# Kernel tuning notes

Measured on AMD Instinct MI355X. Metric: run time of the kernel, lower is better.

The kernel has to match this reference:

```python
import jax, jax.numpy as jnp
import numpy as np

BN_EPS = 1e-5


def gcn_conv(x, src, dst, n, W, b):
    # PyG GCNConv: h = x @ W; add self-loops; symmetric deg^{-1/2} norm; scatter-add; + bias
    h = x @ W
    sl = jnp.arange(n, dtype=src.dtype)
    src_f = jnp.concatenate([src, sl])
    dst_f = jnp.concatenate([dst, sl])
    deg = jax.ops.segment_sum(jnp.ones_like(dst_f, dtype=h.dtype), dst_f, num_segments=n)
    dis = jnp.where(deg > 0, jax.lax.rsqrt(jnp.maximum(deg, 1.0)), 0.0)
    norm = dis[src_f] * dis[dst_f]                       # [E+N]
    msg = h[src_f] * norm[:, None]                       # gather + scale
    out = jax.ops.segment_sum(msg, dst_f, num_segments=n)  # scatter-add
    return out + b


def batchnorm(x, g, b):
    # training-mode BatchNorm1d (batch statistics), deterministic
    mu = jnp.mean(x, axis=0)
    var = jnp.mean((x - mu) ** 2, axis=0)
    return g * (x - mu) * jax.lax.rsqrt(var + BN_EPS) + b


def setup_inputs() -> dict:
    key = jax.random.key(0)
    ks = jax.random.split(key, 12)
    N, E, F_IN, D, M, G = 40000, 640000, 128, 128, 256, 2000
    x = jax.random.normal(ks[0], (N, F_IN), dtype=jnp.float32)
    edge_index = jax.random.randint(ks[1], (2, E), 0, N, dtype=jnp.int64)
    batch = jnp.sort(jax.random.randint(ks[2], (N,), 0, G, dtype=jnp.int64))
    s = lambda fi: 1.0 / np.sqrt(fi)
    W1 = jax.random.normal(ks[3], (F_IN, D), dtype=jnp.float32) * s(F_IN)
    b1 = jnp.zeros((D,), jnp.float32)
    W2 = jax.random.normal(ks[4], (D, D), dtype=jnp.float32) * s(D)
    b2 = jnp.zeros((D,), jnp.float32)
    bn1_g = jnp.ones((D,), jnp.float32); bn1_b = jnp.zeros((D,), jnp.float32)
    bn2_g = jnp.ones((D,), jnp.float32); bn2_b = jnp.zeros((D,), jnp.float32)
    fc1_w = jax.random.normal(ks[5], (D, M), dtype=jnp.float32) * s(D)
    fc1_b = jnp.zeros((M,), jnp.float32)
    fc2_w = jax.random.normal(ks[6], (M, M), dtype=jnp.float32) * s(M)
    fc2_b = jnp.zeros((M,), jnp.float32)
    fc3_w = jax.random.normal(ks[7], (M, 1), dtype=jnp.float32) * s(M)
    fc3_b = jnp.zeros((1,), jnp.float32)
    return dict(x=x, edge_index=edge_index, batch=batch, num_graphs=G,
                W1=W1, b1=b1, W2=W2, b2=b2,
                bn1_g=bn1_g, bn1_b=bn1_b, bn2_g=bn2_g, bn2_b=bn2_b,
                fc1_w=fc1_w, fc1_b=fc1_b, fc2_w=fc2_w, fc2_b=fc2_b,
                fc3_w=fc3_w, fc3_b=fc3_b)


def reference(x, edge_index, batch, num_graphs, W1, b1, W2, b2,
              bn1_g, bn1_b, bn2_g, bn2_b,
              fc1_w, fc1_b, fc2_w, fc2_b, fc3_w, fc3_b):
    n = x.shape[0]
    src, dst = edge_index[0], edge_index[1]
    h = gcn_conv(x, src, dst, n, W1, b1)
    h = jax.nn.relu(batchnorm(h, bn1_g, bn1_b))
    h = gcn_conv(h, src, dst, n, W2, b2)
    h = jax.nn.relu(batchnorm(h, bn2_g, bn2_b))
    g = jax.ops.segment_sum(h, batch, num_segments=num_graphs)  # scatter_sum pooling [G, D]
    g = jax.nn.relu(g @ fc1_w + fc1_b)   # dropout is identity in eval
    g = jax.nn.relu(g @ fc2_w + fc2_b)
    return g @ fc3_w + fc3_b             # [G, 1]
```

## Files before the change

kernel.cpp:

```cpp
#include <hip/hip_runtime.h>
#include <hip/hip_fp16.h>

#define NN 40000
#define NE 640000
#define DF 128
#define NG 2000
#define NCH 157
#define CNTB 625
#define G1_BLKS 313
#define NDPAD 40192

typedef unsigned int u32;
typedef __attribute__((ext_vector_type(8))) short short8;
typedef __attribute__((ext_vector_type(4))) float floatx4;

__device__ inline float2 bf2_to_f2(u32 u) {
    return make_float2(__uint_as_float(u << 16), __uint_as_float(u & 0xffff0000u));
}
__device__ inline u32 f_to_bf(float f) {
    u32 u = __float_as_uint(f);
    return (u + 0x7fffu + ((u >> 16) & 1u)) >> 16;
}
__device__ inline u32 pack_bf2(float a, float b) {
    return f_to_bf(a) | (f_to_bf(b) << 16);
}
__device__ inline float bf_to_f(short s) {
    return __uint_as_float(((u32)(unsigned short)s) << 16);
}
__device__ inline float colw_to_f(int cw) {
    return __half2float(__ushort_as_half((unsigned short)((u32)cw >> 16)));
}

template<bool BF16IN, bool FUSE_BN, bool WT_F32, bool TILE128>
__device__ __forceinline__ void gemm_core(const void* __restrict__ Xv, const void* __restrict__ wsrc,
                                          u32* __restrict__ outb, const float* __restrict__ slots,
                                          const float* __restrict__ gam, const float* __restrict__ bet,
                                          int bid, char* sbuf, float* sc, float* sh) {
    unsigned short* wlds = (unsigned short*)sbuf;
    unsigned short* clds = (unsigned short*)sbuf;
    int tid = threadIdx.x;
    int row0 = bid * (TILE128 ? 128 : 64);

    if (FUSE_BN) {
        if (tid < 128) {
            float s = 0.f, q = 0.f;
            for (int k = 0; k < 64; k++) {
                s += slots[k * 256 + tid];
                q += slots[k * 256 + 128 + tid];
            }
            const float inv_n = 1.0f / (float)NN;
            float mu = s * inv_n;
            float va = fmaf(-mu, mu, q * inv_n);
            float a = gam[tid] * rsqrtf(va + 1e-5f);
            sc[tid] = a;
            sh[tid] = fmaf(-mu, a, bet[tid]);
        }
    }
    if (WT_F32) {
        const float* W = (const float*)wsrc;
        for (int i = tid; i < 16384; i += 256) {
            int k = i >> 7, c = i & 127;
            wlds[c * 136 + k] = (unsigned short)f_to_bf(W[i]);
        }
    } else {
        const unsigned short* wt = (const unsigned short*)wsrc;
        for (int i = tid; i < 2048; i += 256) {
            int c = i >> 4, s = i & 15;
            *(uint4*)&wlds[c * 136 + s * 8] = ((const uint4*)wt)[i];
        }
    }
    __syncthreads();

    int lane = tid & 63;
    int wave = tid >> 6;
    int qr = lane >> 4;
    int rl = lane & 15;

    if (TILE128) {
        int rA0 = row0 + wave * 32 + rl;
        int rA1 = rA0 + 16;
        int rA0c = rA0 < NN ? rA0 : NN - 1;
        int rA1c = rA1 < NN ? rA1 : NN - 1;
        floatx4 acc[2][8];
#pragma unroll
        for (int a = 0; a < 2; a++)
#pragma unroll
            for (int b = 0; b < 8; b++) acc[a][b] = (floatx4){0.f, 0.f, 0.f, 0.f};
#pragma unroll
        for (int kb = 0; kb < 4; kb++) {
            int k0 = kb * 32 + qr * 8;
            short8 a0, a1;
            if (!BF16IN) {
                const float* p0 = (const float*)Xv + (size_t)rA0c * DF + k0;
                const float* p1 = (const float*)Xv + (size_t)rA1c * DF + k0;
                float4 u0 = *(const float4*)p0, u1 = *(const float4*)(p0 + 4);
                float4 v0 = *(const float4*)p1, v1 = *(const float4*)(p1 + 4);
                float fa[8] = {u0.x, u0.y, u0.z, u0.w, u1.x, u1.y, u1.z, u1.w};
                float fb[8] = {v0.x, v0.y, v0.z, v0.w, v1.x, v1.y, v1.z, v1.w};
#pragma unroll
                for (int j = 0; j < 8; j++) { a0[j] = (short)f_to_bf(fa[j]); a1[j] = (short)f_to_bf(fb[j]); }
            } else {
                a0 = *(const short8*)((const u32*)Xv + (size_t)rA0c * 64 + (k0 >> 1));
                a1 = *(const short8*)((const u32*)Xv + (size_t)rA1c * 64 + (k0 >> 1));
                if (FUSE_BN) {
#pragma unroll
                    for (int j = 0; j < 8; j++) {
                        float f0 = fmaxf(fmaf(bf_to_f(a0[j]), sc[k0 + j], sh[k0 + j]), 0.f);
                        float f1 = fmaxf(fmaf(bf_to_f(a1[j]), sc[k0 + j], sh[k0 + j]), 0.f);
                        a0[j] = (short)f_to_bf(f0);
                        a1[j] = (short)f_to_bf(f1);
                    }
                }
            }
#pragma unroll
            for (int ct = 0; ct < 8; ct++) {
                short8 bfr = *(const short8*)&wlds[(ct * 16 + rl) * 136 + k0];
                acc[0][ct] = __builtin_amdgcn_mfma_f32_16x16x32_bf16(a0, bfr, acc[0][ct], 0, 0, 0);
                acc[1][ct] = __builtin_amdgcn_mfma_f32_16x16x32_bf16(a1, bfr, acc[1][ct], 0, 0, 0);
            }
        }
        __syncthreads();
#pragma unroll
        for (int rt = 0; rt < 2; rt++)
#pragma unroll
            for (int ct = 0; ct < 8; ct++)
#pragma unroll
                for (int r = 0; r < 4; r++) {
                    int lr = wave * 32 + rt * 16 + qr * 4 + r;
                    int c = ct * 16 + rl;
                    clds[lr * 136 + c] = (unsigned short)f_to_bf(acc[rt][ct][r]);
                }
        __syncthreads();
        for (int i = tid; i < 2048; i += 256) {
            int lr = i >> 4, s = i & 15;
            int grow = row0 + lr;
            if (grow < NN) {
                uint4 v = *(const uint4*)&clds[lr * 136 + s * 8];
                ((uint4*)(outb + (size_t)grow * 64))[s] = v;
            }
        }
    } else {
        int rA = row0 + wave * 16 + rl;
        floatx4 acc[8];
#pragma unroll
        for (int b = 0; b < 8; b++) acc[b] = (floatx4){0.f, 0.f, 0.f, 0.f};
#pragma unroll
        for (int kb = 0; kb < 4; kb++) {
            int k0 = kb * 32 + qr * 8;
            short8 a0;
            if (!BF16IN) {
                const float* p0 = (const float*)Xv + (size_t)rA * DF + k0;
                float4 u0 = *(const float4*)p0, u1 = *(const float4*)(p0 + 4);
                float fa[8] = {u0.x, u0.y, u0.z, u0.w, u1.x, u1.y, u1.z, u1.w};
#pragma unroll
                for (int j = 0; j < 8; j++) a0[j] = (short)f_to_bf(fa[j]);
            } else {
                a0 = *(const short8*)((const u32*)Xv + (size_t)rA * 64 + (k0 >> 1));
                if (FUSE_BN) {
#pragma unroll
                    for (int j = 0; j < 8; j++) {
                        float f0 = fmaxf(fmaf(bf_to_f(a0[j]), sc[k0 + j], sh[k0 + j]), 0.f);
                        a0[j] = (short)f_to_bf(f0);
                    }
                }
            }
#pragma unroll
            for (int ct = 0; ct < 8; ct++) {
                short8 bfr = *(const short8*)&wlds[(ct * 16 + rl) * 136 + k0];
                acc[ct] = __builtin_amdgcn_mfma_f32_16x16x32_bf16(a0, bfr, acc[ct], 0, 0, 0);
            }
        }
        __syncthreads();
#pragma unroll
        for (int ct = 0; ct < 8; ct++)
#pragma unroll
            for (int r = 0; r < 4; r++) {
                int lr = wave * 16 + qr * 4 + r;
                int c = ct * 16 + rl;
                clds[lr * 136 + c] = (unsigned short)f_to_bf(acc[ct][r]);
            }
        __syncthreads();
        for (int i = tid; i < 1024; i += 256) {
            int lr = i >> 4, s = i & 15;
            uint4 v = *(const uint4*)&clds[lr * 136 + s * 8];
            ((uint4*)(outb + (size_t)(row0 + lr) * 64))[s] = v;
        }
    }
}

__global__ __launch_bounds__(256, 4) void k_countgemm(const int* __restrict__ dst,
                                                      int* __restrict__ deg, float* __restrict__ slots0,
                                                      const float* __restrict__ W1, const float* __restrict__ W2,
                                                      unsigned short* __restrict__ wt2,
                                                      const float* __restrict__ X, u32* __restrict__ outb) {
    __shared__ __align__(16) char sbuf[34816];
    __shared__ float sc[128], sh[128];
    int bid = blockIdx.x;
    int tid = threadIdx.x;
    if (bid < CNTB) {
        int i4 = bid * 256 + tid;
        int4 d4 = ((const int4*)dst)[i4];
        atomicAdd(&deg[d4.x], 1);
        atomicAdd(&deg[d4.y], 1);
        atomicAdd(&deg[d4.z], 1);
        atomicAdd(&deg[d4.w], 1);
        return;
    }
    if (bid < CNTB + 2) {
        float* s = slots0 + (size_t)(bid - CNTB) * 64 * 256;
        for (int i = tid; i < 64 * 256; i += 256) s[i] = 0.f;
        return;
    }
    if (bid == CNTB + 2) {
        for (int i = tid; i < 128 * 128; i += 256) {
            int k = i >> 7, cc = i & 127;
            wt2[cc * 128 + k] = (unsigned short)f_to_bf(W2[i]);
        }
        return;
    }
    gemm_core<false, false, true, true>(X, W1, outb, nullptr, nullptr, nullptr,
                                        bid - CNTB - 3, sbuf, sc, sh);
}

__global__ __launch_bounds__(256) void k_scan(const int* __restrict__ deg,
                                              int* __restrict__ row_ptr, int* __restrict__ curs,
                                              float* __restrict__ dis) {
    __shared__ int red[256];
    __shared__ int ls[256];
    int tid = threadIdx.x;
    int wnd = blockIdx.x;
    int part = 0;
    int lim = wnd * 256;
    for (int idx = tid; idx < lim; idx += 256) part += deg[idx];
    red[tid] = part;
    int n = lim + tid;
    int d = deg[n];
    ls[tid] = d;
    __syncthreads();
#pragma unroll
    for (int off = 128; off > 0; off >>= 1) {
        if (tid < off) red[tid] += red[tid + off];
        __syncthreads();
    }
    int base = red[0];
#pragma unroll
    for (int off = 1; off < 256; off <<= 1) {
        int t = (tid >= off) ? ls[tid - off] : 0;
        __syncthreads();
        ls[tid] += t;
        __syncthreads();
    }
    if (n < NN) {
        int r = base + ls[tid] - d;
        row_ptr[n] = r;
        curs[n] = r;
        dis[n] = rsqrtf((float)(d + 1));
    }
    if (wnd == NCH - 1 && tid == 0) row_ptr[NN] = NE;
}

__global__ __launch_bounds__(256) void k_fill(const int* __restrict__ src, const int* __restrict__ dst,
                                              int* __restrict__ curs,
                                              const float* __restrict__ dis, u32* __restrict__ col) {
    int i4 = blockIdx.x * 256 + threadIdx.x;
    int4 d4 = ((const int4*)dst)[i4];
    int4 s4 = ((const int4*)src)[i4];
    int dd[4] = {d4.x, d4.y, d4.z, d4.w};
    int ss[4] = {s4.x, s4.y, s4.z, s4.w};
#pragma unroll
    for (int q = 0; q < 4; q++) {
        u32 h = (u32)__half_as_ushort(__float2half(dis[ss[q]]));
        int slot = atomicAdd(&curs[dd[q]], 1);
        col[slot] = (u32)ss[q] | (h << 16);
    }
}

__global__ __launch_bounds__(256, 4) void k_gemm2(const u32* __restrict__ Hb, const unsigned short* __restrict__ wt2,
                                                  u32* __restrict__ outb, const float* __restrict__ slots,
                                                  const float* __restrict__ gam, const float* __restrict__ bet) {
    __shared__ __align__(16) char sbuf[34816];
    __shared__ float sc[128], sh[128];
    gemm_core<true, true, false, true>(Hb, wt2, outb, slots, gam, bet, blockIdx.x, sbuf, sc, sh);
}

__global__ __launch_bounds__(256, 8) void k_gather(const u32* __restrict__ Hb, const int* __restrict__ row_ptr,
                                                   const u32* __restrict__ col, const float* __restrict__ dis,
                                                   const float* __restrict__ bias, u32* __restrict__ outb,
                                                   float* __restrict__ slots) {
    __shared__ float sred[4][128];
    __shared__ float qred[4][128];
    int t = threadIdx.x & 63;
    int wv = threadIdx.x >> 6;
    int node = blockIdx.x * 4 + wv;
    float di = dis[node];
    int lo = row_ptr[node], hi = row_ptr[node + 1];
    float2 acc;
    {
        float2 a = bf2_to_f2(Hb[(size_t)node * 64 + t]);
        acc = make_float2(a.x * di, a.y * di);
    }
    for (int base = lo; base < hi; base += 64) {
        int m = hi - base; if (m > 64) m = 64;
        int cw = 0;
        if (t < m) cw = (int)col[base + t];
        int ng = (m + 3) >> 2;
        int c[4]; u32 u[4];
#pragma unroll
        for (int q = 0; q < 4; q++) {
            int idx = q < m ? q : 0;
            c[q] = __shfl(cw, idx);
            u[q] = Hb[(size_t)(c[q] & 0xffff) * 64 + t];
        }
        for (int g = 1; g < ng; g++) {
            int c2[4]; u32 u2[4];
#pragma unroll
            for (int q = 0; q < 4; q++) {
                int ii = g * 4 + q;
                int idx = ii < m ? ii : 0;
                c2[q] = __shfl(cw, idx);
                u2[q] = Hb[(size_t)(c2[q] & 0xffff) * 64 + t];
            }
#pragma unroll
            for (int q = 0; q < 4; q++) {
                int ii = (g - 1) * 4 + q;
                float wq = ii < m ? colw_to_f(c[q]) : 0.f;
                float2 h = bf2_to_f2(u[q]);
                acc.x = fmaf(h.x, wq, acc.x);
                acc.y = fmaf(h.y, wq, acc.y);
            }
#pragma unroll
            for (int q = 0; q < 4; q++) { c[q] = c2[q]; u[q] = u2[q]; }
        }
#pragma unroll
        for (int q = 0; q < 4; q++) {
            int ii = (ng - 1) * 4 + q;
            float wq = ii < m ? colw_to_f(c[q]) : 0.f;
            float2 h = bf2_to_f2(u[q]);
            acc.x = fmaf(h.x, wq, acc.x);
            acc.y = fmaf(h.y, wq, acc.y);
        }
    }
    float2 b = ((const float2*)bias)[t];
    acc.x = fmaf(acc.x, di, b.x);
    acc.y = fmaf(acc.y, di, b.y);
    outb[(size_t)node * 64 + t] = pack_bf2(acc.x, acc.y);
    sred[wv][2 * t] = acc.x;     sred[wv][2 * t + 1] = acc.y;
    qred[wv][2 * t] = acc.x * acc.x; qred[wv][2 * t + 1] = acc.y * acc.y;
    __syncthreads();
    int tid = threadIdx.x;
    if (tid < 128) {
        float s = sred[0][tid] + sred[1][tid] + sred[2][tid] + sred[3][tid];
        float q = qred[0][tid] + qred[1][tid] + qred[2][tid] + qred[3][tid];
        int slot = blockIdx.x & 63;
        atomicAdd(&slots[slot * 256 + tid], s);
        atomicAdd(&slots[slot * 256 + 128 + tid], q);
    }
}

__global__ __launch_bounds__(256) void k_poolfc(const u32* __restrict__ Hb, const int* __restrict__ batch,
                                                const float* __restrict__ slots,
                                                const float* __restrict__ gam, const float* __restrict__ bet,
                                                const float* __restrict__ fc1w, const float* __restrict__ fc1b,
                                                const float* __restrict__ fc2w, const float* __restrict__ fc2b,
                                                const float* __restrict__ fc3w, const float* __restrict__ fc3b,
                                                float* __restrict__ out) {
    __shared__ float sc[128], sh[128];
    __shared__ float pooled[4][128];
    __shared__ float g1[4][256];
    __shared__ float g2[4][256];
    __shared__ int bnds[5];
    int tid = threadIdx.x;
    int gbase = blockIdx.x * 4;
    if (tid < 128) {
        float s = 0.f, q = 0.f;
        for (int k = 0; k < 64; k++) {
            s += slots[k * 256 + tid];
            q += slots[k * 256 + 128 + tid];
        }
        const float inv_n = 1.0f / (float)NN;
        float mu = s * inv_n;
        float va = fmaf(-mu, mu, q * inv_n);
        float a = gam[tid] * rsqrtf(va + 1e-5f);
        sc[tid] = a;
        sh[tid] = fmaf(-mu, a, bet[tid]);
    } else if (tid < 133) {
        int target = gbase + (tid - 128);
        int a = 0, b = NN;
        while (a < b) { int m = (a + b) >> 1; if (batch[m] < target) a = m + 1; else b = m; }
        bnds[tid - 128] = a;
    }
    __syncthreads();
    {
        int g = tid >> 6, p = tid & 63;
        int lo = bnds[g], hi = bnds[g + 1];
        float a0 = 0.f, a1 = 0.f;
        float sc0 = sc[2 * p], sh0 = sh[2 * p], sc1 = sc[2 * p + 1], sh1 = sh[2 * p + 1];
        for (int i = lo; i < hi; i++) {
            float2 v = bf2_to_f2(Hb[(size_t)i * 64 + p]);
            a0 += fmaxf(fmaf(v.x, sc0, sh0), 0.f);
            a1 += fmaxf(fmaf(v.y, sc1, sh1), 0.f);
        }
        pooled[g][2 * p] = a0;
        pooled[g][2 * p + 1] = a1;
    }
    __syncthreads();
    {
        float x0 = 0.f, x1 = 0.f, x2 = 0.f, x3 = 0.f;
        for (int k = 0; k < 128; k++) {
            float wv = fc1w[k * 256 + tid];
            x0 = fmaf(pooled[0][k], wv, x0);
            x1 = fmaf(pooled[1][k], wv, x1);
            x2 = fmaf(pooled[2][k], wv, x2);
            x3 = fmaf(pooled[3][k], wv, x3);
        }
        float bb = fc1b[tid];
        g1[0][tid] = fmaxf(x0 + bb, 0.f);
        g1[1][tid] = fmaxf(x1 + bb, 0.f);
        g1[2][tid] = fmaxf(x2 + bb, 0.f);
        g1[3][tid] = fmaxf(x3 + bb, 0.f);
    }
    __syncthreads();
    {
        float x0 = 0.f, x1 = 0.f, x2 = 0.f, x3 = 0.f;
        for (int k = 0; k < 256; k++) {
            float wv = fc2w[k * 256 + tid];
            x0 = fmaf(g1[0][k], wv, x0);
            x1 = fmaf(g1[1][k], wv, x1);
            x2 = fmaf(g1[2][k], wv, x2);
            x3 = fmaf(g1[3][k], wv, x3);
        }
        float bb = fc2b[tid];
        g2[0][tid] = fmaxf(x0 + bb, 0.f);
        g2[1][tid] = fmaxf(x1 + bb, 0.f);
        g2[2][tid] = fmaxf(x2 + bb, 0.f);
        g2[3][tid] = fmaxf(x3 + bb, 0.f);
    }
    __syncthreads();
    {
        int lane = tid & 63, wv = tid >> 6;
        float s = fmaf(g2[wv][lane], fc3w[lane],
                  fmaf(g2[wv][64 + lane], fc3w[64 + lane],
                  fmaf(g2[wv][128 + lane], fc3w[128 + lane],
                       g2[wv][192 + lane] * fc3w[192 + lane])));
        for (int off = 32; off > 0; off >>= 1) s += __shfl_down(s, off);
        if (lane == 0) out[gbase + wv] = s + fc3b[0];
    }
}

extern "C" void kernel_launch(void* const* d_in, const int* in_sizes, int n_in,
                              void* d_out, int out_size, void* d_ws, size_t ws_size,
                              hipStream_t stream) {
    const float* x    = (const float*)d_in[0];
    const int*   ei   = (const int*)d_in[1];
    const int*   batch= (const int*)d_in[2];
    const float* W1   = (const float*)d_in[4];
    const float* b1   = (const float*)d_in[5];
    const float* W2   = (const float*)d_in[6];
    const float* b2   = (const float*)d_in[7];
    const float* bn1g = (const float*)d_in[8];
    const float* bn1b = (const float*)d_in[9];
    const float* bn2g = (const float*)d_in[10];
    const float* bn2b = (const float*)d_in[11];
    const float* fc1w = (const float*)d_in[12];
    const float* fc1b = (const float*)d_in[13];
    const float* fc2w = (const float*)d_in[14];
    const float* fc2b = (const float*)d_in[15];
    const float* fc3w = (const float*)d_in[16];
    const float* fc3b = (const float*)d_in[17];
    const int* src = ei;
    const int* dst = ei + NE;
    float* outp = (float*)d_out;

    char* w = (char*)d_ws;
    size_t o = 0;
    auto alloc = [&](size_t bytes) -> char* {
        char* p = w + o;
        o = (o + bytes + 255) & ~(size_t)255;
        return p;
    };
    int*   deg     = (int*)alloc((size_t)NDPAD * 4);
    int*   curs    = (int*)alloc((size_t)NDPAD * 4);
    float* slots0  = (float*)alloc((size_t)2 * 64 * 256 * 4);
    int*   row_ptr = (int*)alloc((size_t)(NN + 1) * 4);
    u32*   col     = (u32*)alloc((size_t)NE * 4);
    float* dis     = (float*)alloc((size_t)NN * 4);
    unsigned short* wt2 = (unsigned short*)alloc(128 * 128 * 2);
    u32*   bufA    = (u32*)alloc((size_t)NN * 64 * 4);
    u32*   bufB    = (u32*)alloc((size_t)NN * 64 * 4);
    float* slotsA  = slots0;
    float* slotsB  = slots0 + 64 * 256;

    hipMemsetAsync(deg, 0, (size_t)NDPAD * 4, stream);
    k_countgemm<<<CNTB + 3 + G1_BLKS, 256, 0, stream>>>(dst, deg, slots0, W1, W2, wt2, x, bufA);
    k_scan<<<NCH, 256, 0, stream>>>(deg, row_ptr, curs, dis);
    k_fill<<<CNTB, 256, 0, stream>>>(src, dst, curs, dis, col);
    k_gather<<<NN / 4, 256, 0, stream>>>(bufA, row_ptr, col, dis, b1, bufB, slotsA);
    k_gemm2<<<G1_BLKS, 256, 0, stream>>>(bufB, wt2, bufA, slotsA, bn1g, bn1b);
    k_gather<<<NN / 4, 256, 0, stream>>>(bufA, row_ptr, col, dis, b2, bufB, slotsB);
    k_poolfc<<<NG / 4, 256, 0, stream>>>(bufB, batch, slotsB, bn2g, bn2b,
                                         fc1w, fc1b, fc2w, fc2b, fc3w, fc3b, outp);
}
```

Measured before the change: 287.9 us.

## Pre-transpose weights in a prep kernel, use XOR-swizzled LDS, 64-row GEMM tiles

Adds a k_prep kernel that zeroes the BN stat slots and degree array and converts W1 and W2 to transposed bf16. This replaces the memset and the per-block fp32 weight conversion that every GEMM1 block used to repeat. Both GEMMs now use 64-row tiles (625 blocks) instead of 128-row tiles, and the LDS layout switches from a padded 136 stride to an XOR swizzle, which shrinks shared memory and raises the occupancy hint to 5. The trade-off is an extra kernel launch and twice as many blocks, each reloading the weights into LDS.

```diff
diff --git a/kernel.cpp b/kernel.cpp
--- a/kernel.cpp
+++ b/kernel.cpp
@@ -7,7 +7,7 @@
 #define NG 2000
 #define NCH 157
 #define CNTB 625
-#define G1_BLKS 313
+#define GT_BLKS 625
 #define NDPAD 40192
 
 typedef unsigned int u32;
@@ -31,15 +31,15 @@
     return __half2float(__ushort_as_half((unsigned short)((u32)cw >> 16)));
 }
 
-template<bool BF16IN, bool FUSE_BN, bool WT_F32, bool TILE128>
-__device__ __forceinline__ void gemm_core(const void* __restrict__ Xv, const void* __restrict__ wsrc,
+template<bool BF16IN, bool FUSE_BN>
+__device__ __forceinline__ void gemm_core(const void* __restrict__ Xv, const unsigned short* __restrict__ wt,
                                           u32* __restrict__ outb, const float* __restrict__ slots,
                                           const float* __restrict__ gam, const float* __restrict__ bet,
                                           int bid, char* sbuf, float* sc, float* sh) {
     unsigned short* wlds = (unsigned short*)sbuf;
     unsigned short* clds = (unsigned short*)sbuf;
     int tid = threadIdx.x;
-    int row0 = bid * (TILE128 ? 128 : 64);
+    int row0 = bid * 64;
 
     if (FUSE_BN) {
         if (tid < 128) {
@@ -56,18 +56,9 @@
             sh[tid] = fmaf(-mu, a, bet[tid]);
         }
     }
-    if (WT_F32) {
-        const float* W = (const float*)wsrc;
-        for (int i = tid; i < 16384; i += 256) {
-            int k = i >> 7, c = i & 127;
-            wlds[c * 136 + k] = (unsigned short)f_to_bf(W[i]);
-        }
-    } else {
-        const unsigned short* wt = (const unsigned short*)wsrc;
-        for (int i = tid; i < 2048; i += 256) {
-            int c = i >> 4, s = i & 15;
-            *(uint4*)&wlds[c * 136 + s * 8] = ((const uint4*)wt)[i];
-        }
+    for (int i = tid; i < 2048; i += 256) {
+        int c = i >> 4, s = i & 15;
+        *(uint4*)&wlds[c * 128 + ((s ^ (c & 7)) << 3)] = ((const uint4*)wt)[i];
     }
     __syncthreads();
 
@@ -76,125 +67,82 @@
     int qr = lane >> 4;
     int rl = lane & 15;
 
-    if (TILE128) {
-        int rA0 = row0 + wave * 32 + rl;
-        int rA1 = rA0 + 16;
-        int rA0c = rA0 < NN ? rA0 : NN - 1;
-        int rA1c = rA1 < NN ? rA1 : NN - 1;
-        floatx4 acc[2][8];
-#pragma unroll
-        for (int a = 0; a < 2; a++)
-#pragma unroll
-            for (int b = 0; b < 8; b++) acc[a][b] = (floatx4){0.f, 0.f, 0.f, 0.f};
-#pragma unroll
-        for (int kb = 0; kb < 4; kb++) {
-            int k0 = kb * 32 + qr * 8;
-            short8 a0, a1;
-            if (!BF16IN) {
-                const float* p0 = (const float*)Xv + (size_t)rA0c * DF + k0;
-                const float* p1 = (const float*)Xv + (size_t)rA1c * DF + k0;
-                float4 u0 = *(const float4*)p0, u1 = *(const float4*)(p0 + 4);
-                float4 v0 = *(const float4*)p1, v1 = *(const float4*)(p1 + 4);
-                float fa[8] = {u0.x, u0.y, u0.z, u0.w, u1.x, u1.y, u1.z, u1.w};
-                float fb[8] = {v0.x, v0.y, v0.z, v0.w, v1.x, v1.y, v1.z, v1.w};
-#pragma unroll
-                for (int j = 0; j < 8; j++) { a0[j] = (short)f_to_bf(fa[j]); a1[j] = (short)f_to_bf(fb[j]); }
-            } else {
-                a0 = *(const short8*)((const u32*)Xv + (size_t)rA0c * 64 + (k0 >> 1));
-                a1 = *(const short8*)((const u32*)Xv + (size_t)rA1c * 64 + (k0 >> 1));
-                if (FUSE_BN) {
-#pragma unroll
-                    for (int j = 0; j < 8; j++) {
-                        float f0 = fmaxf(fmaf(bf_to_f(a0[j]), sc[k0 + j], sh[k0 + j]), 0.f);
-                        float f1 = fmaxf(fmaf(bf_to_f(a1[j]), sc[k0 + j], sh[k0 + j]), 0.f);
-                        a0[j] = (short)f_to_bf(f0);
-                        a1[j] = (short)f_to_bf(f1);
-                    }
+    int rA = row0 + wave * 16 + rl;
+    floatx4 acc[8];
+#pragma unroll
+    for (int b = 0; b < 8; b++) acc[b] = (floatx4){0.f, 0.f, 0.f, 0.f};
+#pragma unroll
+    for (int kb = 0; kb < 4; kb++) {
+        int k0 = kb * 32 + qr * 8;
+        short8 a0;
+        if (!BF16IN) {
+            const float* p0 = (const float*)Xv + (size_t)rA * DF + k0;
+            float4 u0 = *(const float4*)p0, u1 = *(const float4*)(p0 + 4);
+            float fa[8] = {u0.x, u0.y, u0.z, u0.w, u1.x, u1.y, u1.z, u1.w};
+#pragma unroll
+            for (int j = 0; j < 8; j++) a0[j] = (short)f_to_bf(fa[j]);
+        } else {
+            a0 = *(const short8*)((const u32*)Xv + (size_t)rA * 64 + (k0 >> 1));
+            if (FUSE_BN) {
+#pragma unroll
+                for (int j = 0; j < 8; j++) {
+                    float f0 = fmaxf(fmaf(bf_to_f(a0[j]), sc[k0 + j], sh[k0 + j]), 0.f);
+                    a0[j] = (short)f_to_bf(f0);
                 }
             }
-#pragma unroll
-            for (int ct = 0; ct < 8; ct++) {
-                short8 bfr = *(const short8*)&wlds[(ct * 16 + rl) * 136 + k0];
-                acc[0][ct] = __builtin_amdgcn_mfma_f32_16x16x32_bf16(a0, bfr, acc[0][ct], 0, 0, 0);
-                acc[1][ct] = __builtin_amdgcn_mfma_f32_16x16x32_bf16(a1, bfr, acc[1][ct], 0, 0, 0);
-            }
-        }
-        __syncthreads();
-#pragma unroll
-        for (int rt = 0; rt < 2; rt++)
-#pragma unroll
-            for (int ct = 0; ct < 8; ct++)
-#pragma unroll
-                for (int r = 0; r < 4; r++) {
-                    int lr = wave * 32 + rt * 16 + qr * 4 + r;
-                    int c = ct * 16 + rl;
-                    clds[lr * 136 + c] = (unsigned short)f_to_bf(acc[rt][ct][r]);
-                }
-        __syncthreads();
-        for (int i = tid; i < 2048; i += 256) {
-            int lr = i >> 4, s = i & 15;
-            int grow = row0 + lr;
-            if (grow < NN) {
-                uint4 v = *(const uint4*)&clds[lr * 136 + s * 8];
-                ((uint4*)(outb + (size_t)grow * 64))[s] = v;
-            }
-        }
+        }
+#pragma unroll
+        for (int ct = 0; ct < 8; ct++) {
+            int rowB = ct * 16 + rl;
+            short8 bfr = *(const short8*)&wlds[rowB * 128 + ((((kb << 2) + qr) ^ (rl & 7)) << 3)];
+            acc[ct] = __builtin_amdgcn_mfma_f32_16x16x32_bf16(a0, bfr, acc[ct], 0, 0, 0);
+        }
+    }
+    __syncthreads();
+#pragma unroll
+    for (int ct = 0; ct < 8; ct++)
+#pragma unroll
+        for (int r = 0; r < 4; r++) {
+            int lr = wave * 16 + qr * 4 + r;
+            int c = ct * 16 + rl;
+            clds[lr * 128 + (((c >> 3) ^ (lr & 7)) << 3) + (c & 7)] = (unsigned short)f_to_bf(acc[ct][r]);
+        }
+    __syncthreads();
+    for (int i = tid; i < 1024; i += 256) {
+        int lr = i >> 4, s = i & 15;
+        uint4 v = *(const uint4*)&clds[lr * 128 + ((s ^ (lr & 7)) << 3)];
+        ((uint4*)(outb + (size_t)(row0 + lr) * 64))[s] = v;
+    }
+}
+
+__global__ __launch_bounds__(256) void k_prep(const float* __restrict__ W1, const float* __restrict__ W2,
+                                              unsigned short* __restrict__ wt1, unsigned short* __restrict__ wt2,
+                                              float* __restrict__ slots0, int* __restrict__ deg) {
+    int bid = blockIdx.x, tid = threadIdx.x;
+    if (bid < 64) {
+        slots0[bid * 512 + tid] = 0.f;
+        slots0[bid * 512 + 256 + tid] = 0.f;
+    } else if (bid < 104) {
+        int i = (bid - 64) * 1024 + tid;
+#pragma unroll
+        for (int q = 0; q < 4; q++) {
+            int j = i + q * 256;
+            if (j < NDPAD) deg[j] = 0;
+        }
+    } else if (bid < 168) {
+        int i = (bid - 104) * 256 + tid;
+        wt1[i] = (unsigned short)f_to_bf(W1[(i & 127) * 128 + (i >> 7)]);
     } else {
-        int rA = row0 + wave * 16 + rl;
-        floatx4 acc[8];
-#pragma unroll
-        for (int b = 0; b < 8; b++) acc[b] = (floatx4){0.f, 0.f, 0.f, 0.f};
-#pragma unroll
-        for (int kb = 0; kb < 4; kb++) {
-            int k0 = kb * 32 + qr * 8;
-            short8 a0;
-            if (!BF16IN) {
-                const float* p0 = (const float*)Xv + (size_t)rA * DF + k0;
-                float4 u0 = *(const float4*)p0, u1 = *(const float4*)(p0 + 4);
-                float fa[8] = {u0.x, u0.y, u0.z, u0.w, u1.x, u1.y, u1.z, u1.w};
-#pragma unroll
-                for (int j = 0; j < 8; j++) a0[j] = (short)f_to_bf(fa[j]);
-            } else {
-                a0 = *(const short8*)((const u32*)Xv + (size_t)rA * 64 + (k0 >> 1));
-                if (FUSE_BN) {
-#pragma unroll
-                    for (int j = 0; j < 8; j++) {
-                        float f0 = fmaxf(fmaf(bf_to_f(a0[j]), sc[k0 + j], sh[k0 + j]), 0.f);
-                        a0[j] = (short)f_to_bf(f0);
-                    }
-                }
-            }
-#pragma unroll
-            for (int ct = 0; ct < 8; ct++) {
-                short8 bfr = *(const short8*)&wlds[(ct * 16 + rl) * 136 + k0];
-                acc[ct] = __builtin_amdgcn_mfma_f32_16x16x32_bf16(a0, bfr, acc[ct], 0, 0, 0);
-            }
-        }
-        __syncthreads();
-#pragma unroll
-        for (int ct = 0; ct < 8; ct++)
-#pragma unroll
-            for (int r = 0; r < 4; r++) {
-                int lr = wave * 16 + qr * 4 + r;
-                int c = ct * 16 + rl;
-                clds[lr * 136 + c] = (unsigned short)f_to_bf(acc[ct][r]);
-            }
-        __syncthreads();
-        for (int i = tid; i < 1024; i += 256) {
-            int lr = i >> 4, s = i & 15;
-            uint4 v = *(const uint4*)&clds[lr * 136 + s * 8];
-            ((uint4*)(outb + (size_t)(row0 + lr) * 64))[s] = v;
-        }
-    }
-}
-
-__global__ __launch_bounds__(256, 4) void k_countgemm(const int* __restrict__ dst,
-                                                      int* __restrict__ deg, float* __restrict__ slots0,
-                                                      const float* __restrict__ W1, const float* __restrict__ W2,
-                                                      unsigned short* __restrict__ wt2,
+        int i = (bid - 168) * 256 + tid;
+        wt2[i] = (unsigned short)f_to_bf(W2[(i & 127) * 128 + (i >> 7)]);
+    }
+}
+
+__global__ __launch_bounds__(256, 5) void k_countgemm(const int* __restrict__ dst,
+                                                      int* __restrict__ deg,
+                                                      const unsigned short* __restrict__ wt1,
                                                       const float* __restrict__ X, u32* __restrict__ outb) {
-    __shared__ __align__(16) char sbuf[34816];
-    __shared__ float sc[128], sh[128];
+    __shared__ __align__(16) char sbuf[32768];
     int bid = blockIdx.x;
     int tid = threadIdx.x;
     if (bid < CNTB) {
@@ -206,20 +154,8 @@
         atomicAdd(&deg[d4.w], 1);
         return;
     }
-    if (bid < CNTB + 2) {
-        float* s = slots0 + (size_t)(bid - CNTB) * 64 * 256;
-        for (int i = tid; i < 64 * 256; i += 256) s[i] = 0.f;
-        return;
-    }
-    if (bid == CNTB + 2) {
-        for (int i = tid; i < 128 * 128; i += 256) {
-            int k = i >> 7, cc = i & 127;
-            wt2[cc * 128 + k] = (unsigned short)f_to_bf(W2[i]);
-        }
-        return;
-    }
-    gemm_core<false, false, true, true>(X, W1, outb, nullptr, nullptr, nullptr,
-                                        bid - CNTB - 3, sbuf, sc, sh);
+    gemm_core<false, false>(X, wt1, outb, nullptr, nullptr, nullptr,
+                            bid - CNTB, sbuf, nullptr, nullptr);
 }
 
 __global__ __launch_bounds__(256) void k_scan(const int* __restrict__ deg,
@@ -278,9 +214,9 @@
 __global__ __launch_bounds__(256, 4) void k_gemm2(const u32* __restrict__ Hb, const unsigned short* __restrict__ wt2,
                                                   u32* __restrict__ outb, const float* __restrict__ slots,
                                                   const float* __restrict__ gam, const float* __restrict__ bet) {
-    __shared__ __align__(16) char sbuf[34816];
+    __shared__ __align__(16) char sbuf[32768];
     __shared__ float sc[128], sh[128];
-    gemm_core<true, true, false, true>(Hb, wt2, outb, slots, gam, bet, blockIdx.x, sbuf, sc, sh);
+    gemm_core<true, true>(Hb, wt2, outb, slots, gam, bet, blockIdx.x, sbuf, sc, sh);
 }
 
 __global__ __launch_bounds__(256, 8) void k_gather(const u32* __restrict__ Hb, const int* __restrict__ row_ptr,
@@ -484,18 +420,19 @@
     int*   row_ptr = (int*)alloc((size_t)(NN + 1) * 4);
     u32*   col     = (u32*)alloc((size_t)NE * 4);
     float* dis     = (float*)alloc((size_t)NN * 4);
+    unsigned short* wt1 = (unsigned short*)alloc(128 * 128 * 2);
     unsigned short* wt2 = (unsigned short*)alloc(128 * 128 * 2);
     u32*   bufA    = (u32*)alloc((size_t)NN * 64 * 4);
     u32*   bufB    = (u32*)alloc((size_t)NN * 64 * 4);
     float* slotsA  = slots0;
     float* slotsB  = slots0 + 64 * 256;
 
-    hipMemsetAsync(deg, 0, (size_t)NDPAD * 4, stream);
-    k_countgemm<<<CNTB + 3 + G1_BLKS, 256, 0, stream>>>(dst, deg, slots0, W1, W2, wt2, x, bufA);
+    k_prep<<<232, 256, 0, stream>>>(W1, W2, wt1, wt2, slots0, deg);
+    k_countgemm<<<CNTB + GT_BLKS, 256, 0, stream>>>(dst, deg, wt1, x, bufA);
     k_scan<<<NCH, 256, 0, stream>>>(deg, row_ptr, curs, dis);
     k_fill<<<CNTB, 256, 0, stream>>>(src, dst, curs, dis, col);
     k_gather<<<NN / 4, 256, 0, stream>>>(bufA, row_ptr, col, dis, b1, bufB, slotsA);
-    k_gemm2<<<G1_BLKS, 256, 0, stream>>>(bufB, wt2, bufA, slotsA, bn1g, bn1b);
+    k_gemm2<<<GT_BLKS, 256, 0, stream>>>(bufB, wt2, bufA, slotsA, bn1g, bn1b);
     k_gather<<<NN / 4, 256, 0, stream>>>(bufA, row_ptr, col, dis, b2, bufB, slotsB);
     k_poolfc<<<NG / 4, 256, 0, stream>>>(bufB, batch, slotsB, bn2g, bn2b,
                                          fc1w, fc1b, fc2w, fc2b, fc3w, fc3b, outp);
```

Result: faster. 280.2 us (-2.7%).
